# Kernel tuning notes

Hardware: AMD Instinct MI355X
Metric: run time of the kernel (lower is better)

Reference implementation:

```python
import jax, jax.numpy as jnp
import numpy as np

B, L, N = 16, 512, 512
DM, DS, NL, DFF = 512, 16, 2, 2048
DI = 2 * DM          # expand=2
DCONV = 4
DTR = DM // 16       # dt_rank
H = 96
EPS = 1e-5


def _ln(x, w, b):
    m = jnp.mean(x, -1, keepdims=True)
    v = jnp.mean((x - m) ** 2, -1, keepdims=True)
    return (x - m) / jnp.sqrt(v + EPS) * w + b


def _mamba_dir(x, in_w, in_b, conv_w, conv_b, xp_w, dt_w, dt_b, A_log, Dp, out_w, out_b):
    # x: (B, S, DM)
    Bb, S, _ = x.shape
    xz = x @ in_w.T + in_b                       # (B,S,2*DI)
    u, z = jnp.split(xz, 2, -1)
    uc = jnp.swapaxes(u, 1, 2)                   # (B,DI,S)
    uc = jax.lax.conv_general_dilated(uc, conv_w[:, None, :], (1,), [(DCONV - 1, 0)],
                                      feature_group_count=DI,
                                      dimension_numbers=('NCH', 'OIH', 'NCH'))
    u = jax.nn.silu(jnp.swapaxes(uc + conv_b[None, :, None], 1, 2))  # (B,S,DI)
    x_dbl = u @ xp_w.T                           # (B,S,DTR+2*DS)
    dt, Bm, Cm = jnp.split(x_dbl, [DTR, DTR + DS], -1)
    delta = jax.nn.softplus(dt @ dt_w.T + dt_b)  # (B,S,DI)
    A = -jnp.exp(A_log)                          # (DI,DS)

    def step(h, inp):
        u_t, d_t, B_t, C_t = inp                 # (B,DI),(B,DI),(B,DS),(B,DS)
        h = jnp.exp(d_t[:, :, None] * A) * h + (d_t * u_t)[:, :, None] * B_t[:, None, :]
        return h, jnp.einsum('bds,bs->bd', h, C_t)

    h0 = jnp.zeros((Bb, DI, DS), x.dtype)
    _, ys = jax.lax.scan(step, h0, (jnp.swapaxes(u, 0, 1), jnp.swapaxes(delta, 0, 1),
                                    jnp.swapaxes(Bm, 0, 1), jnp.swapaxes(Cm, 0, 1)))
    y = jnp.swapaxes(ys, 0, 1) + u * Dp          # (B,S,DI)
    y = y * jax.nn.silu(z)
    return y @ out_w.T + out_b                   # (B,S,DM)


def _forward(x, tok_w, tok_b, in_w, in_b, conv_w, conv_b, xp_w, dt_w, dt_b, A_log, Dm,
             out_w, out_b, mnorm_w, mnorm_b, fnorm_w, fnorm_b, ffn_w1, ffn_b1, ffn_w2,
             ffn_b2, norm_w, norm_b, head_w, head_b):
    # RevIN: per-instance stats over time dim, no affine
    mu = jnp.mean(x, 1, keepdims=True)           # (B,1,N)
    sd = jnp.sqrt(jnp.var(x, 1, keepdims=True) + EPS)
    xn = (x - mu) / sd
    tokens = jnp.swapaxes(xn, 1, 2) @ tok_w.T + tok_b   # (B,N,DM) variate tokens
    for l in range(NL):
        yn = _ln(tokens, mnorm_w[l], mnorm_b[l])
        of = _mamba_dir(yn, in_w[l, 0], in_b[l, 0], conv_w[l, 0], conv_b[l, 0], xp_w[l, 0],
                        dt_w[l, 0], dt_b[l, 0], A_log[l, 0], Dm[l, 0], out_w[l, 0], out_b[l, 0])
        ob = _mamba_dir(yn[:, ::-1, :], in_w[l, 1], in_b[l, 1], conv_w[l, 1], conv_b[l, 1],
                        xp_w[l, 1], dt_w[l, 1], dt_b[l, 1], A_log[l, 1], Dm[l, 1],
                        out_w[l, 1], out_b[l, 1])[:, ::-1, :]
        tokens = tokens + of + ob                # bidirectional Mamba + residual
        res = tokens
        hdd = _ln(tokens, fnorm_w[l], fnorm_b[l])
        hdd = jax.nn.gelu(hdd @ ffn_w1[l].T + ffn_b1[l]) @ ffn_w2[l].T + ffn_b2[l]
        tokens = hdd + res
    tokens = _ln(tokens, norm_w, norm_b)
    pred = tokens @ head_w.T + head_b            # (B,N,H)
    pred = jnp.swapaxes(pred, 1, 2)              # (B,H,N)
    return pred * sd + mu                        # RevIN inverse


def setup_inputs() -> dict:
    key = jax.random.key(0)
    ks = jax.random.split(key, 12)
    def rn(k, shape, scale=0.02):
        return jax.random.normal(k, shape, jnp.float32) * scale
    return {
        'x': jax.random.normal(ks[0], (B, L, N), jnp.float32),
        'tok_w': rn(ks[1], (DM, L)), 'tok_b': jnp.zeros((DM,), jnp.float32),
        'in_w': rn(ks[2], (NL, 2, 2 * DI, DM)), 'in_b': jnp.zeros((NL, 2, 2 * DI), jnp.float32),
        'conv_w': rn(ks[3], (NL, 2, DI, DCONV), 0.2), 'conv_b': jnp.zeros((NL, 2, DI), jnp.float32),
        'xp_w': rn(ks[4], (NL, 2, DTR + 2 * DS, DI)),
        'dt_w': rn(ks[5], (NL, 2, DI, DTR)), 'dt_b': rn(ks[6], (NL, 2, DI), 0.1),
        'A_log': jnp.broadcast_to(jnp.log(jnp.arange(1., DS + 1.)), (NL, 2, DI, DS)).astype(jnp.float32),
        'Dm': jnp.ones((NL, 2, DI), jnp.float32),
        'out_w': rn(ks[7], (NL, 2, DM, DI)), 'out_b': jnp.zeros((NL, 2, DM), jnp.float32),
        'mnorm_w': jnp.ones((NL, DM), jnp.float32), 'mnorm_b': jnp.zeros((NL, DM), jnp.float32),
        'fnorm_w': jnp.ones((NL, DM), jnp.float32), 'fnorm_b': jnp.zeros((NL, DM), jnp.float32),
        'ffn_w1': rn(ks[8], (NL, DFF, DM)), 'ffn_b1': jnp.zeros((NL, DFF), jnp.float32),
        'ffn_w2': rn(ks[9], (NL, DM, DFF)), 'ffn_b2': jnp.zeros((NL, DM), jnp.float32),
        'norm_w': jnp.ones((DM,), jnp.float32), 'norm_b': jnp.zeros((DM,), jnp.float32),
        'head_w': rn(ks[10], (H, DM)), 'head_b': jnp.zeros((H,), jnp.float32),
    }


def reference(x, tok_w, tok_b, in_w, in_b, conv_w, conv_b, xp_w, dt_w, dt_b, A_log, Dm,
              out_w, out_b, mnorm_w, mnorm_b, fnorm_w, fnorm_b, ffn_w1, ffn_b1, ffn_w2,
              ffn_b2, norm_w, norm_b, head_w, head_b):
    return _forward(x, tok_w, tok_b, in_w, in_b, conv_w, conv_b, xp_w, dt_w, dt_b, A_log,
                    Dm, out_w, out_b, mnorm_w, mnorm_b, fnorm_w, fnorm_b, ffn_w1, ffn_b1,
                    ffn_w2, ffn_b2, norm_w, norm_b, head_w, head_b)
```

## Files before the change

### kernel.cpp

```cpp
#include <hip/hip_runtime.h>
#include <hip/hip_bf16.h>

#define Bb 16
#define Ll 512
#define NV 512
#define DM 512
#define DS 16
#define NLAY 2
#define DFF 2048
#define DI 1024
#define DCONV 4
#define DTR 32
#define Hh 96
#define Ss NV
#define MROWS (Bb*Ss)
#define EPSf 1e-5f
#define CH 64
#define NCH (Ss/CH)

typedef __hip_bfloat16 bf16;
typedef __attribute__((ext_vector_type(8))) short bf16x8;
typedef __attribute__((ext_vector_type(4))) float f32x4;

#define GLL16(g, l) __builtin_amdgcn_global_load_lds( \
    (const __attribute__((address_space(1))) unsigned int*)(g), \
    (__attribute__((address_space(3))) unsigned int*)(l), 16, 0, 0)

__device__ __forceinline__ float fast_exp(float x) { return __expf(x); }
__device__ __forceinline__ float fast_sig(float x) {
    return __builtin_amdgcn_rcpf(1.f + __expf(-x));
}
__device__ __forceinline__ float fast_softplus(float r) {
    float e = __expf(-fabsf(r));
    return fmaxf(r, 0.f) + __logf(1.f + e);
}
__device__ __forceinline__ float b2f(bf16 v) { return __bfloat162float(v); }

__global__ void f2bf(const float* __restrict__ in, bf16* __restrict__ out, int n) {
    int i = (blockIdx.x * 256 + threadIdx.x) * 4;
    if (i < n) {
        float4 v = *(const float4*)(in + i);
        out[i + 0] = __float2bfloat16(v.x);
        out[i + 1] = __float2bfloat16(v.y);
        out[i + 2] = __float2bfloat16(v.z);
        out[i + 3] = __float2bfloat16(v.w);
    }
}

__global__ void repack_outw(const float* __restrict__ outw, bf16* __restrict__ outwcat) {
    int idx = (blockIdx.x * 256 + threadIdx.x) * 4;
    int k2 = idx & 2047;
    int rest = idx >> 11;
    int l = rest >> 9, n = rest & 511;
    int dirk = k2 >> 10, k = k2 & 1023;
    const float* s = outw + (((size_t)(l * 2 + dirk) * DM + n) * DI + k);
    float4 v = *(const float4*)s;
    bf16* dpt = outwcat + (size_t)idx;
    dpt[0] = __float2bfloat16(v.x);
    dpt[1] = __float2bfloat16(v.y);
    dpt[2] = __float2bfloat16(v.z);
    dpt[3] = __float2bfloat16(v.w);
}

__global__ void sum_outb(const float* __restrict__ outb, float* __restrict__ outbsum) {
    int i = blockIdx.x * 256 + threadIdx.x;
    int l = i >> 9, n = i & 511;
    outbsum[i] = outb[(l * 2 + 0) * DM + n] + outb[(l * 2 + 1) * DM + n];
}

__global__ void build_xpw2(const float* __restrict__ xpw, bf16* __restrict__ out) {
    int idx = blockIdx.x * 256 + threadIdx.x;
    int l = idx >> 18;
    int rest = idx & 262143;
    int n = rest >> 11, k = rest & 2047;
    int dir = n >> 6, nn = n & 63;
    float v = ((k >> 10) == dir) ? xpw[((size_t)(l * 2 + dir) * 64 + nn) * DI + (k & 1023)] : 0.f;
    out[idx] = __float2bfloat16(v);
}

__global__ void build_dtw2(const float* __restrict__ dtw, bf16* __restrict__ out) {
    int idx = blockIdx.x * 256 + threadIdx.x;
    int l = idx >> 18;
    int rest = idx & 262143;
    int n = rest >> 7, k = rest & 127;
    int dir = n >> 10, nn = n & 1023;
    int r = k - dir * 64;
    float v = (r >= 0 && r < DTR) ? dtw[((size_t)(l * 2 + dir) * DI + nn) * DTR + r] : 0.f;
    out[idx] = __float2bfloat16(v);
}

__global__ void revin_partial(const float* __restrict__ x, float* __restrict__ ps1,
                              float* __restrict__ ps2) {
    int b = blockIdx.x, c = blockIdx.y, n = threadIdx.x;
    const float* xp = x + (size_t)b * Ll * NV + (size_t)c * (Ll / 8) * NV + n;
    float s1 = 0.f, s2 = 0.f;
    #pragma unroll 4
    for (int l = 0; l < Ll / 8; l++) { float v = xp[(size_t)l * NV]; s1 += v; s2 += v * v; }
    ps1[((size_t)b * 8 + c) * NV + n] = s1;
    ps2[((size_t)b * 8 + c) * NV + n] = s2;
}

__global__ void revin_final(const float* __restrict__ ps1, const float* __restrict__ ps2,
                            float* __restrict__ mu, float* __restrict__ sd) {
    int b = blockIdx.x, n = threadIdx.x;
    float s1 = 0.f, s2 = 0.f;
    #pragma unroll
    for (int c = 0; c < 8; c++) {
        s1 += ps1[((size_t)b * 8 + c) * NV + n];
        s2 += ps2[((size_t)b * 8 + c) * NV + n];
    }
    float m = s1 / Ll;
    float var = s2 / Ll - m * m;
    mu[b * NV + n] = m;
    sd[b * NV + n] = sqrtf(var + EPSf);
}

__global__ void transpose_norm(const float* __restrict__ x, const float* __restrict__ mu,
                               const float* __restrict__ sd, bf16* __restrict__ xnT) {
    __shared__ float t[32][33];
    int b = blockIdx.z;
    int l0 = blockIdx.x * 32, n0 = blockIdx.y * 32;
    int tx = threadIdx.x, ty = threadIdx.y;
    #pragma unroll
    for (int q = 0; q < 4; q++)
        t[ty + q * 8][tx] = x[(size_t)b * Ll * NV + (size_t)(l0 + ty + q * 8) * NV + n0 + tx];
    __syncthreads();
    #pragma unroll
    for (int q = 0; q < 4; q++) {
        int n = n0 + ty + q * 8;
        float m = mu[b * NV + n], s = sd[b * NV + n];
        xnT[(size_t)b * NV * Ll + (size_t)n * Ll + l0 + tx] = __float2bfloat16((t[tx][ty + q * 8] - m) / s);
    }
}

__global__ void ln_rows(const float* __restrict__ in, const float* __restrict__ w,
                        const float* __restrict__ bvec, bf16* __restrict__ out) {
    int row = blockIdx.x;
    int tid = threadIdx.x;
    float v = in[(size_t)row * DM + tid];
    float s1 = v, s2 = v * v;
    #pragma unroll
    for (int o = 32; o > 0; o >>= 1) { s1 += __shfl_down(s1, o, 64); s2 += __shfl_down(s2, o, 64); }
    __shared__ float l1[8], l2[8];
    int wv = tid >> 6, ln = tid & 63;
    if (ln == 0) { l1[wv] = s1; l2[wv] = s2; }
    __syncthreads();
    if (tid == 0) {
        float a = 0.f, c = 0.f;
        #pragma unroll
        for (int i = 0; i < DM / 64; i++) { a += l1[i]; c += l2[i]; }
        l1[0] = a; l2[0] = c;
    }
    __syncthreads();
    float mean = l1[0] / DM;
    float var = l2[0] / DM - mean * mean;
    float inv = rsqrtf(var + EPSf);
    out[(size_t)row * DM + tid] = __float2bfloat16((v - mean) * inv * w[tid] + bvec[tid]);
}

template<int EPI, bool ACC, bool OUTBF>
__global__ __launch_bounds__(256) void gemm128(
    const bf16* __restrict__ A, int lda,
    const bf16* __restrict__ W,
    const float* __restrict__ bias,
    void* __restrict__ Cv, int ldc,
    int M, int Nn, int K) {
    __shared__ bf16 As[2][128 * 32];
    __shared__ bf16 Bs[2][128 * 32];
    int m0 = blockIdx.x * 128, n0 = blockIdx.y * 128;
    int tid = threadIdx.x;
    int w = tid >> 6, lane = tid & 63;
    int wm = (w >> 1) * 64, wn = (w & 1) * 64;
    f32x4 acc[4][4] = {};

    int srow = w * 32 + (lane >> 2);
    int sslot = (lane & 3) ^ ((lane >> 3) & 3);
    long arow0 = m0 + srow, arow1 = m0 + srow + 16;
    const char* agp0 = (const char*)(A + arow0 * (long)lda) + sslot * 16;
    const char* agp1 = (const char*)(A + arow1 * (long)lda) + sslot * 16;
    long wr0 = n0 + srow;      if (wr0 >= Nn) wr0 = Nn - 1;
    long wr1 = n0 + srow + 16; if (wr1 >= Nn) wr1 = Nn - 1;
    const char* wgp0 = (const char*)(W + wr0 * (long)K) + sslot * 16;
    const char* wgp1 = (const char*)(W + wr1 * (long)K) + sslot * 16;

    char* a0 = (char*)As[0]; char* a1 = (char*)As[1];
    char* b0 = (char*)Bs[0]; char* b1 = (char*)Bs[1];
    int dA0 = (w * 32) * 64, dA1 = (w * 32 + 16) * 64;

    int lrow = lane & 15;
    int salt = ((lane >> 4) ^ ((lane >> 1) & 3)) * 16;

    const int nk = K >> 5;
#define STG128(pa, pb, ko) do { \
        GLL16(agp0 + (size_t)(ko) * 64, pa + dA0); \
        GLL16(agp1 + (size_t)(ko) * 64, pa + dA1); \
        GLL16(wgp0 + (size_t)(ko) * 64, pb + dA0); \
        GLL16(wgp1 + (size_t)(ko) * 64, pb + dA1); } while (0)

    STG128(a0, b0, 0);
    __syncthreads();
    for (int t = 0; t < nk; ++t) {
        char* ac = (t & 1) ? a1 : a0;
        char* bc = (t & 1) ? b1 : b0;
        if (t + 1 < nk) {
            char* an = (t & 1) ? a0 : a1;
            char* bn = (t & 1) ? b0 : b1;
            STG128(an, bn, t + 1);
        }
        bf16x8 af[4], bfr[4];
        #pragma unroll
        for (int i = 0; i < 4; i++) {
            af[i]  = *(const bf16x8*)(ac + (wm + i * 16 + lrow) * 64 + salt);
            bfr[i] = *(const bf16x8*)(bc + (wn + i * 16 + lrow) * 64 + salt);
        }
        #pragma unroll
        for (int i = 0; i < 4; i++)
            #pragma unroll
            for (int j = 0; j < 4; j++)
                acc[i][j] = __builtin_amdgcn_mfma_f32_16x16x32_bf16(af[i], bfr[j], acc[i][j], 0, 0, 0);
        __syncthreads();
    }
#undef STG128

    #pragma unroll
    for (int i = 0; i < 4; i++) {
        #pragma unroll
        for (int j = 0; j < 4; j++) {
            int n = n0 + wn + j * 16 + (lane & 15);
            if (n >= Nn) continue;
            float bv = bias ? bias[n] : 0.f;
            #pragma unroll
            for (int r = 0; r < 4; r++) {
                long m = m0 + wm + i * 16 + (lane >> 4) * 4 + r;
                float v = acc[i][j][r] + bv;
                if (EPI == 1) {
                    float x3 = v * v * v;
                    v = 0.5f * v * (1.f + tanhf(0.7978845608028654f * (v + 0.044715f * x3)));
                }
                if (OUTBF) {
                    ((bf16*)Cv)[m * (long)ldc + n] = __float2bfloat16(v);
                } else if (ACC) {
                    ((float*)Cv)[m * (long)ldc + n] += v;
                } else {
                    ((float*)Cv)[m * (long)ldc + n] = v;
                }
            }
        }
    }
}

template<int EPI, bool ACC, bool OUTBF, int MT>
__global__ __launch_bounds__(256) void gemm64(
    const bf16* __restrict__ A, int lda,
    const bf16* __restrict__ W,
    const float* __restrict__ bias,
    void* __restrict__ Cv, int ldc,
    int M, int Nn, int K) {
    constexpr int WR = MT / 4;
    constexpr int IF = MT / 64;
    constexpr int AG = WR / 8;
    __shared__ bf16 As[2][MT * 64];
    __shared__ bf16 Bs[2][64 * 64];
    int m0 = blockIdx.x * MT, n0 = blockIdx.y * 64;
    int tid = threadIdx.x;
    int w = tid >> 6, lane = tid & 63;
    int wm = w * WR;
    f32x4 acc[IF][4] = {};

    int srow = lane >> 3;
    int sslot = (lane & 7) ^ srow;
    const char* agp[AG];
    #pragma unroll
    for (int g = 0; g < AG; g++) {
        long ar = m0 + w * WR + g * 8 + srow;
        agp[g] = (const char*)(A + ar * (long)lda) + sslot * 16;
    }
    const char* wgp[2];
    #pragma unroll
    for (int g = 0; g < 2; g++) {
        long br = n0 + w * 16 + g * 8 + srow;
        if (br >= Nn) br = Nn - 1;
        wgp[g] = (const char*)(W + br * (long)K) + sslot * 16;
    }
    char* a0 = (char*)As[0]; char* a1 = (char*)As[1];
    char* b0 = (char*)Bs[0]; char* b1 = (char*)Bs[1];

    int lrow = lane & 15;
    int rk = lane & 7, hi = lane >> 4;
    int salt0 = (hi ^ rk) * 16;
    int salt1 = ((4 + hi) ^ rk) * 16;

    const int nk = K >> 6;
#define STG64(pa, pb, ko) do { \
        _Pragma("unroll") \
        for (int g = 0; g < AG; g++) \
            GLL16(agp[g] + (size_t)(ko) * 128, pa + (w * WR + g * 8) * 128); \
        _Pragma("unroll") \
        for (int g = 0; g < 2; g++) \
            GLL16(wgp[g] + (size_t)(ko) * 128, pb + (w * 16 + g * 8) * 128); } while (0)

    STG64(a0, b0, 0);
    __syncthreads();
    for (int t = 0; t < nk; ++t) {
        char* ac = (t & 1) ? a1 : a0;
        char* bc = (t & 1) ? b1 : b0;
        if (t + 1 < nk) {
            char* an = (t & 1) ? a0 : a1;
            char* bn = (t & 1) ? b0 : b1;
            STG64(an, bn, t + 1);
        }
        bf16x8 af[2][IF], bfr[2][4];
        #pragma unroll
        for (int i = 0; i < IF; i++) {
            af[0][i] = *(const bf16x8*)(ac + (wm + i * 16 + lrow) * 128 + salt0);
            af[1][i] = *(const bf16x8*)(ac + (wm + i * 16 + lrow) * 128 + salt1);
        }
        #pragma unroll
        for (int j = 0; j < 4; j++) {
            bfr[0][j] = *(const bf16x8*)(bc + (j * 16 + lrow) * 128 + salt0);
            bfr[1][j] = *(const bf16x8*)(bc + (j * 16 + lrow) * 128 + salt1);
        }
        #pragma unroll
        for (int kk = 0; kk < 2; kk++)
            #pragma unroll
            for (int i = 0; i < IF; i++)
                #pragma unroll
                for (int j = 0; j < 4; j++)
                    acc[i][j] = __builtin_amdgcn_mfma_f32_16x16x32_bf16(af[kk][i], bfr[kk][j], acc[i][j], 0, 0, 0);
        __syncthreads();
    }
#undef STG64

    #pragma unroll
    for (int i = 0; i < IF; i++) {
        #pragma unroll
        for (int j = 0; j < 4; j++) {
            int n = n0 + j * 16 + (lane & 15);
            if (n >= Nn) continue;
            float bv = bias ? bias[n] : 0.f;
            #pragma unroll
            for (int r = 0; r < 4; r++) {
                long m = m0 + wm + i * 16 + (lane >> 4) * 4 + r;
                float v = acc[i][j][r] + bv;
                if (EPI == 1) {
                    float x3 = v * v * v;
                    v = 0.5f * v * (1.f + tanhf(0.7978845608028654f * (v + 0.044715f * x3)));
                } else if (EPI == 2) {
                    v = fast_softplus(v);
                }
                if (OUTBF) {
                    ((bf16*)Cv)[m * (long)ldc + n] = __float2bfloat16(v);
                } else if (ACC) {
                    ((float*)Cv)[m * (long)ldc + n] += v;
                } else {
                    ((float*)Cv)[m * (long)ldc + n] = v;
                }
            }
        }
    }
}

__global__ void conv_both(const bf16* __restrict__ xz, const float* __restrict__ cw_l,
                          const float* __restrict__ cb_l, bf16* __restrict__ ub) {
    int c2 = blockIdx.x * 256 + threadIdx.x;
    int dir = c2 >> 10, c = c2 & 1023;
    int s0 = blockIdx.y * 16;
    int b = blockIdx.z;
    const bf16* src = xz + (size_t)b * Ss * 4096 + (size_t)dir * 2048 + c;
    const float* cw = cw_l + (dir * DI + c) * 4;
    float w0 = cw[0], w1 = cw[1], w2 = cw[2], w3 = cw[3];
    float bias = cb_l[dir * DI + c];
    bf16* dst = ub + (size_t)b * Ss * 2048 + (size_t)dir * 1024 + c;
    if (dir == 0) {
        float r0 = (s0 - 3 >= 0) ? b2f(src[(size_t)(s0 - 3) * 4096]) : 0.f;
        float r1 = (s0 - 2 >= 0) ? b2f(src[(size_t)(s0 - 2) * 4096]) : 0.f;
        float r2 = (s0 - 1 >= 0) ? b2f(src[(size_t)(s0 - 1) * 4096]) : 0.f;
        for (int i = 0; i < 16; i++) {
            int s = s0 + i;
            float r3 = b2f(src[(size_t)s * 4096]);
            float a = fmaf(r0, w0, fmaf(r1, w1, fmaf(r2, w2, fmaf(r3, w3, bias))));
            dst[(size_t)s * 2048] = __float2bfloat16(a * fast_sig(a));
            r0 = r1; r1 = r2; r2 = r3;
        }
    } else {
        float f0 = b2f(src[(size_t)s0 * 4096]);
        float f1 = (s0 + 1 < Ss) ? b2f(src[(size_t)(s0 + 1) * 4096]) : 0.f;
        float f2 = (s0 + 2 < Ss) ? b2f(src[(size_t)(s0 + 2) * 4096]) : 0.f;
        float f3 = (s0 + 3 < Ss) ? b2f(src[(size_t)(s0 + 3) * 4096]) : 0.f;
        for (int i = 0; i < 16; i++) {
            int s = s0 + i;
            float a = fmaf(f0, w3, fmaf(f1, w2, fmaf(f2, w1, fmaf(f3, w0, bias))));
            dst[(size_t)s * 2048] = __float2bfloat16(a * fast_sig(a));
            f0 = f1; f1 = f2; f2 = f3;
            f3 = (s + 4 < Ss) ? b2f(src[(size_t)(s + 4) * 4096]) : 0.f;
        }
    }
}

__global__ __launch_bounds__(256) void scan_pass1(
    const bf16* __restrict__ delb,
    const bf16* __restrict__ ub,
    const float* __restrict__ xd,
    const float* __restrict__ Alog_l,
    float* __restrict__ PB, float* __restrict__ HB) {
    int d2 = blockIdx.x * 256 + threadIdx.x;
    int dir = d2 >> 10, d = d2 & 1023;
    int c = blockIdx.y;
    int b = blockIdx.z;
    float Aj[DS], h[DS];
    const float* al = Alog_l + ((size_t)dir * DI + d) * DS;
    #pragma unroll
    for (int j = 0; j < DS; j++) { Aj[j] = -fast_exp(al[j]); h[j] = 0.f; }
    float dlsum = 0.f;
    for (int i = 0; i < CH; i++) {
        int t = c * CH + i;
        int p = dir ? (Ss - 1 - t) : t;
        size_t row = (size_t)b * Ss + p;
        float dl = b2f(delb[row * 2048 + d2]);
        float ut = b2f(ub[row * 2048 + d2]);
        float du = dl * ut;
        dlsum += dl;
        const float4* q4 = (const float4*)(xd + row * 128 + dir * 64 + DTR);
        float4 B0 = q4[0], B1 = q4[1], B2 = q4[2], B3 = q4[3];
        float Bv[DS] = {B0.x, B0.y, B0.z, B0.w, B1.x, B1.y, B1.z, B1.w,
                        B2.x, B2.y, B2.z, B2.w, B3.x, B3.y, B3.z, B3.w};
        #pragma unroll
        for (int j = 0; j < DS; j++) {
            float a = fast_exp(dl * Aj[j]);
            h[j] = fmaf(a, h[j], du * Bv[j]);
        }
    }
    size_t base = ((size_t)(b * NCH + c) * DS) * 2048 + d2;
    #pragma unroll
    for (int j = 0; j < DS; j++) {
        PB[base + (size_t)j * 2048] = fast_exp(dlsum * Aj[j]);
        HB[base + (size_t)j * 2048] = h[j];
    }
}

__global__ __launch_bounds__(256) void scan_pass2(
    const float* PB, const float* HB, float* HIN) {
    int idx = blockIdx.x * 256 + threadIdx.x;
    int b = idx >> 15;
    int rem = idx & 32767;
    float h = 0.f;
    #pragma unroll
    for (int c = 0; c < NCH; c++) {
        size_t o = ((size_t)(b * NCH + c)) * 32768 + rem;
        float p = PB[o];
        float hl = HB[o];
        HIN[o] = h;
        h = fmaf(p, h, hl);
    }
}

__global__ __launch_bounds__(256) void scan_pass3(
    const bf16* __restrict__ delb,
    const bf16* __restrict__ ub,
    const float* __restrict__ xd,
    const bf16* __restrict__ xzb,
    const float* __restrict__ Alog_l, const float* __restrict__ Dm_l,
    const float* __restrict__ HIN,
    bf16* __restrict__ yb) {
    int d2 = blockIdx.x * 256 + threadIdx.x;
    int dir = d2 >> 10, d = d2 & 1023;
    int c = blockIdx.y;
    int b = blockIdx.z;
    float Aj[DS], h[DS];
    const float* al = Alog_l + ((size_t)dir * DI + d) * DS;
    size_t hbase = ((size_t)(b * NCH + c) * DS) * 2048 + d2;
    #pragma unroll
    for (int j = 0; j < DS; j++) {
        Aj[j] = -fast_exp(al[j]);
        h[j] = HIN[hbase + (size_t)j * 2048];
    }
    float Dd = Dm_l[dir * DI + d];
    for (int i = 0; i < CH; i++) {
        int t = c * CH + i;
        int p = dir ? (Ss - 1 - t) : t;
        size_t row = (size_t)b * Ss + p;
        float dl = b2f(delb[row * 2048 + d2]);
        float ut = b2f(ub[row * 2048 + d2]);
        float zz = b2f(xzb[row * 4096 + dir * 2048 + 1024 + d]);
        float du = dl * ut;
        const float4* q4 = (const float4*)(xd + row * 128 + dir * 64 + DTR);
        float4 B0 = q4[0], B1 = q4[1], B2 = q4[2], B3 = q4[3];
        float4 C0 = q4[4], C1 = q4[5], C2 = q4[6], C3 = q4[7];
        float Bv[DS] = {B0.x, B0.y, B0.z, B0.w, B1.x, B1.y, B1.z, B1.w,
                        B2.x, B2.y, B2.z, B2.w, B3.x, B3.y, B3.z, B3.w};
        float Cv[DS] = {C0.x, C0.y, C0.z, C0.w, C1.x, C1.y, C1.z, C1.w,
                        C2.x, C2.y, C2.z, C2.w, C3.x, C3.y, C3.z, C3.w};
        float acc = 0.f;
        #pragma unroll
        for (int j = 0; j < DS; j++) {
            float a = fast_exp(dl * Aj[j]);
            h[j] = fmaf(a, h[j], du * Bv[j]);
            acc = fmaf(h[j], Cv[j], acc);
        }
        float sg = fast_sig(zz);
        yb[row * 2048 + d2] = __float2bfloat16((acc + ut * Dd) * (zz * sg));
    }
}

__global__ void finalize_out(const float* __restrict__ pred, const float* __restrict__ mu,
                             const float* __restrict__ sd, float* __restrict__ out) {
    int n = threadIdx.x;
    int h = blockIdx.x;
    int b = blockIdx.y;
    out[((size_t)b * Hh + h) * NV + n] =
        pred[((size_t)b * NV + n) * Hh + h] * sd[b * NV + n] + mu[b * NV + n];
}

extern "C" void kernel_launch(void* const* d_in, const int* in_sizes, int n_in,
                              void* d_out, int out_size, void* d_ws, size_t ws_size,
                              hipStream_t stream) {
    const float* x     = (const float*)d_in[0];
    const float* tokw  = (const float*)d_in[1];
    const float* tokb  = (const float*)d_in[2];
    const float* in_w  = (const float*)d_in[3];
    const float* in_b  = (const float*)d_in[4];
    const float* convw = (const float*)d_in[5];
    const float* convb = (const float*)d_in[6];
    const float* xpw   = (const float*)d_in[7];
    const float* dtw   = (const float*)d_in[8];
    const float* dtb   = (const float*)d_in[9];
    const float* Alog  = (const float*)d_in[10];
    const float* Dm    = (const float*)d_in[11];
    const float* outw  = (const float*)d_in[12];
    const float* outb  = (const float*)d_in[13];
    const float* mnw   = (const float*)d_in[14];
    const float* mnb   = (const float*)d_in[15];
    const float* fnw   = (const float*)d_in[16];
    const float* fnb   = (const float*)d_in[17];
    const float* fw1   = (const float*)d_in[18];
    const float* fb1   = (const float*)d_in[19];
    const float* fw2   = (const float*)d_in[20];
    const float* fb2   = (const float*)d_in[21];
    const float* nw    = (const float*)d_in[22];
    const float* nb    = (const float*)d_in[23];
    const float* hw    = (const float*)d_in[24];
    const float* hb    = (const float*)d_in[25];

    float* ws = (float*)d_ws;
    float* MU   = ws;
    float* SD   = MU + Bb * NV;
    float* R1   = SD + Bb * NV;
    float* T    = R1 + 2 * 1024 * 1024;
    float* YNR  = T + 4 * 1024 * 1024;
    float* XZR  = YNR + 2 * 1024 * 1024;
    float* UBR  = XZR + 16 * 1024 * 1024;
    float* DELR = UBR + 8 * 1024 * 1024;
    float* PB   = DELR + 8 * 1024 * 1024;
    float* HB   = PB + 4 * 1024 * 1024;
    float* YBR  = HB + 4 * 1024 * 1024;
    float* WBF  = YBR + 8 * 1024 * 1024;

    bf16* XNTb = (bf16*)R1;
    float* XD  = R1;
    bf16* XDb  = (bf16*)(R1 + 1024 * 1024);
    bf16* YNb  = (bf16*)YNR;
    bf16* XZb  = (bf16*)XZR;
    bf16* Ub   = (bf16*)UBR;
    bf16* DELb = (bf16*)DELR;
    bf16* Yb   = (bf16*)YBR;
    float* HIN = PB;
    float* PRED = DELR;

    bf16* wb = (bf16*)WBF;
    bf16* tokwb  = wb;  wb += (size_t)DM * Ll;
    bf16* inwb   = wb;  wb += (size_t)NLAY * 2 * 2 * DI * DM;
    bf16* xpw2b  = wb;  wb += (size_t)NLAY * 128 * 2048;
    bf16* dtw2b  = wb;  wb += (size_t)NLAY * 2048 * 128;
    bf16* outwc  = wb;  wb += (size_t)NLAY * DM * 2 * DI;
    bf16* fw1b   = wb;  wb += (size_t)NLAY * DFF * DM;
    bf16* fw2b   = wb;  wb += (size_t)NLAY * DM * DFF;
    bf16* hwb    = wb;  wb += (size_t)Hh * DM;
    float* outbsum = (float*)wb;
    float* PS1   = outbsum + NLAY * DM;
    float* PS2   = PS1 + Bb * 8 * NV;

    f2bf<<<(DM * Ll) / 1024, 256, 0, stream>>>(tokw, tokwb, DM * Ll);
    f2bf<<<(NLAY * 2 * 2 * DI * DM) / 1024, 256, 0, stream>>>(in_w, inwb, NLAY * 2 * 2 * DI * DM);
    build_xpw2<<<(NLAY * 128 * 2048) / 256, 256, 0, stream>>>(xpw, xpw2b);
    build_dtw2<<<(NLAY * 2048 * 128) / 256, 256, 0, stream>>>(dtw, dtw2b);
    repack_outw<<<(NLAY * DM * 2 * DI) / 1024, 256, 0, stream>>>(outw, outwc);
    sum_outb<<<(NLAY * DM) / 256, 256, 0, stream>>>(outb, outbsum);
    f2bf<<<(NLAY * DFF * DM) / 1024, 256, 0, stream>>>(fw1, fw1b, NLAY * DFF * DM);
    f2bf<<<(NLAY * DM * DFF) / 1024, 256, 0, stream>>>(fw2, fw2b, NLAY * DM * DFF);
    f2bf<<<(Hh * DM) / 1024, 256, 0, stream>>>(hw, hwb, Hh * DM);

    revin_partial<<<dim3(Bb, 8), NV, 0, stream>>>(x, PS1, PS2);
    revin_final<<<Bb, NV, 0, stream>>>(PS1, PS2, MU, SD);
    transpose_norm<<<dim3(Ll / 32, NV / 32, Bb), dim3(32, 8), 0, stream>>>(x, MU, SD, XNTb);
    gemm64<0, false, false, 128><<<dim3(MROWS / 128, DM / 64), 256, 0, stream>>>(
        XNTb, Ll, tokwb, tokb, T, DM, MROWS, DM, Ll);

    for (int l = 0; l < NLAY; l++) {
        ln_rows<<<MROWS, DM, 0, stream>>>(T, mnw + l * DM, mnb + l * DM, YNb);
        gemm128<0, false, true><<<dim3(MROWS / 128, 4096 / 128), 256, 0, stream>>>(
            YNb, DM, inwb + (size_t)l * 2 * 2 * DI * DM, in_b + (size_t)l * 2 * 2 * DI,
            XZb, 4096, MROWS, 4096, DM);
        conv_both<<<dim3(8, Ss / 16, Bb), 256, 0, stream>>>(
            XZb, convw + (size_t)l * 2 * DI * DCONV, convb + (size_t)l * 2 * DI, Ub);
        gemm64<0, false, false, 64><<<dim3(MROWS / 64, 2), 256, 0, stream>>>(
            Ub, 2048, xpw2b + (size_t)l * 128 * 2048, nullptr, XD, 128, MROWS, 128, 2048);
        f2bf<<<(MROWS * 128) / 1024, 256, 0, stream>>>(XD, XDb, MROWS * 128);
        gemm64<2, false, true, 128><<<dim3(MROWS / 128, 2048 / 64), 256, 0, stream>>>(
            XDb, 128, dtw2b + (size_t)l * 2048 * 128, dtb + (size_t)l * 2 * DI,
            DELb, 2048, MROWS, 2048, 128);
        scan_pass1<<<dim3(2048 / 256, NCH, Bb), 256, 0, stream>>>(
            DELb, Ub, XD, Alog + (size_t)l * 2 * DI * DS, PB, HB);
        scan_pass2<<<(Bb * DS * 2048) / 256, 256, 0, stream>>>(PB, HB, HIN);
        scan_pass3<<<dim3(2048 / 256, NCH, Bb), 256, 0, stream>>>(
            DELb, Ub, XD, XZb, Alog + (size_t)l * 2 * DI * DS, Dm + (size_t)l * 2 * DI,
            HIN, Yb);
        gemm64<0, true, false, 128><<<dim3(MROWS / 128, DM / 64), 256, 0, stream>>>(
            Yb, 2 * DI, outwc + (size_t)l * DM * 2 * DI, outbsum + l * DM,
            T, DM, MROWS, DM, 2 * DI);
        ln_rows<<<MROWS, DM, 0, stream>>>(T, fnw + l * DM, fnb + l * DM, YNb);
        gemm128<1, false, true><<<dim3(MROWS / 128, DFF / 128), 256, 0, stream>>>(
            YNb, DM, fw1b + (size_t)l * DFF * DM, fb1 + l * DFF, XZb, DFF, MROWS, DFF, DM);
        gemm64<0, true, false, 128><<<dim3(MROWS / 128, DM / 64), 256, 0, stream>>>(
            XZb, DFF, fw2b + (size_t)l * DM * DFF, fb2 + l * DM, T, DM, MROWS, DM, DFF);
    }
    ln_rows<<<MROWS, DM, 0, stream>>>(T, nw, nb, YNb);
    gemm64<0, false, false, 64><<<dim3(MROWS / 64, 2), 256, 0, stream>>>(
        YNb, DM, hwb, hb, PRED, Hh, MROWS, Hh, DM);
    finalize_out<<<dim3(Hh, Bb), NV, 0, stream>>>(PRED, MU, SD, (float*)d_out);
}
```

Baseline: 931.7 us.

## Compute local scan outputs in pass1 and apply carry-in correction per row in pass3

```diff
diff --git a/kernel.cpp b/kernel.cpp
--- a/kernel.cpp
+++ b/kernel.cpp
@@ -45,6 +45,11 @@
         out[i + 2] = __float2bfloat16(v.z);
         out[i + 3] = __float2bfloat16(v.w);
     }
+}
+
+__global__ void a2negA(const float* __restrict__ alog, float* __restrict__ negA, int n) {
+    int i = blockIdx.x * 256 + threadIdx.x;
+    if (i < n) negA[i] = -fast_exp(alog[i]);
 }
 
 __global__ void repack_outw(const float* __restrict__ outw, bf16* __restrict__ outwcat) {
@@ -398,91 +403,35 @@
 }
 
 __global__ __launch_bounds__(256) void scan_pass1(
-    const bf16* __restrict__ delb,
-    const bf16* __restrict__ ub,
+    bf16* __restrict__ delb_dt,
+    bf16* __restrict__ ub_ypre,
     const float* __restrict__ xd,
-    const float* __restrict__ Alog_l,
+    const float* __restrict__ negA_l,
+    const float* __restrict__ Dm_l,
     float* __restrict__ PB, float* __restrict__ HB) {
     int d2 = blockIdx.x * 256 + threadIdx.x;
     int dir = d2 >> 10, d = d2 & 1023;
     int c = blockIdx.y;
     int b = blockIdx.z;
     float Aj[DS], h[DS];
-    const float* al = Alog_l + ((size_t)dir * DI + d) * DS;
-    #pragma unroll
-    for (int j = 0; j < DS; j++) { Aj[j] = -fast_exp(al[j]); h[j] = 0.f; }
+    const float4* na4 = (const float4*)(negA_l + ((size_t)dir * DI + d) * DS);
+    float4 A0 = na4[0], A1 = na4[1], A2 = na4[2], A3 = na4[3];
+    Aj[0]=A0.x; Aj[1]=A0.y; Aj[2]=A0.z; Aj[3]=A0.w;
+    Aj[4]=A1.x; Aj[5]=A1.y; Aj[6]=A1.z; Aj[7]=A1.w;
+    Aj[8]=A2.x; Aj[9]=A2.y; Aj[10]=A2.z; Aj[11]=A2.w;
+    Aj[12]=A3.x; Aj[13]=A3.y; Aj[14]=A3.z; Aj[15]=A3.w;
+    #pragma unroll
+    for (int j = 0; j < DS; j++) h[j] = 0.f;
+    float Dd = Dm_l[dir * DI + d];
     float dlsum = 0.f;
     for (int i = 0; i < CH; i++) {
         int t = c * CH + i;
         int p = dir ? (Ss - 1 - t) : t;
         size_t row = (size_t)b * Ss + p;
-        float dl = b2f(delb[row * 2048 + d2]);
-        float ut = b2f(ub[row * 2048 + d2]);
+        float dl = b2f(delb_dt[row * 2048 + d2]);
+        float ut = b2f(ub_ypre[row * 2048 + d2]);
         float du = dl * ut;
         dlsum += dl;
-        const float4* q4 = (const float4*)(xd + row * 128 + dir * 64 + DTR);
-        float4 B0 = q4[0], B1 = q4[1], B2 = q4[2], B3 = q4[3];
-        float Bv[DS] = {B0.x, B0.y, B0.z, B0.w, B1.x, B1.y, B1.z, B1.w,
-                        B2.x, B2.y, B2.z, B2.w, B3.x, B3.y, B3.z, B3.w};
-        #pragma unroll
-        for (int j = 0; j < DS; j++) {
-            float a = fast_exp(dl * Aj[j]);
-            h[j] = fmaf(a, h[j], du * Bv[j]);
-        }
-    }
-    size_t base = ((size_t)(b * NCH + c) * DS) * 2048 + d2;
-    #pragma unroll
-    for (int j = 0; j < DS; j++) {
-        PB[base + (size_t)j * 2048] = fast_exp(dlsum * Aj[j]);
-        HB[base + (size_t)j * 2048] = h[j];
-    }
-}
-
-__global__ __launch_bounds__(256) void scan_pass2(
-    const float* PB, const float* HB, float* HIN) {
-    int idx = blockIdx.x * 256 + threadIdx.x;
-    int b = idx >> 15;
-    int rem = idx & 32767;
-    float h = 0.f;
-    #pragma unroll
-    for (int c = 0; c < NCH; c++) {
-        size_t o = ((size_t)(b * NCH + c)) * 32768 + rem;
-        float p = PB[o];
-        float hl = HB[o];
-        HIN[o] = h;
-        h = fmaf(p, h, hl);
-    }
-}
-
-__global__ __launch_bounds__(256) void scan_pass3(
-    const bf16* __restrict__ delb,
-    const bf16* __restrict__ ub,
-    const float* __restrict__ xd,
-    const bf16* __restrict__ xzb,
-    const float* __restrict__ Alog_l, const float* __restrict__ Dm_l,
-    const float* __restrict__ HIN,
-    bf16* __restrict__ yb) {
-    int d2 = blockIdx.x * 256 + threadIdx.x;
-    int dir = d2 >> 10, d = d2 & 1023;
-    int c = blockIdx.y;
-    int b = blockIdx.z;
-    float Aj[DS], h[DS];
-    const float* al = Alog_l + ((size_t)dir * DI + d) * DS;
-    size_t hbase = ((size_t)(b * NCH + c) * DS) * 2048 + d2;
-    #pragma unroll
-    for (int j = 0; j < DS; j++) {
-        Aj[j] = -fast_exp(al[j]);
-        h[j] = HIN[hbase + (size_t)j * 2048];
-    }
-    float Dd = Dm_l[dir * DI + d];
-    for (int i = 0; i < CH; i++) {
-        int t = c * CH + i;
-        int p = dir ? (Ss - 1 - t) : t;
-        size_t row = (size_t)b * Ss + p;
-        float dl = b2f(delb[row * 2048 + d2]);
-        float ut = b2f(ub[row * 2048 + d2]);
-        float zz = b2f(xzb[row * 4096 + dir * 2048 + 1024 + d]);
-        float du = dl * ut;
         const float4* q4 = (const float4*)(xd + row * 128 + dir * 64 + DTR);
         float4 B0 = q4[0], B1 = q4[1], B2 = q4[2], B3 = q4[3];
         float4 C0 = q4[4], C1 = q4[5], C2 = q4[6], C3 = q4[7];
@@ -497,9 +446,65 @@
             h[j] = fmaf(a, h[j], du * Bv[j]);
             acc = fmaf(h[j], Cv[j], acc);
         }
-        float sg = fast_sig(zz);
-        yb[row * 2048 + d2] = __float2bfloat16((acc + ut * Dd) * (zz * sg));
-    }
+        ub_ypre[row * 2048 + d2] = __float2bfloat16(acc + ut * Dd);
+        delb_dt[row * 2048 + d2] = __float2bfloat16(dlsum);
+    }
+    size_t base = ((size_t)(b * NCH + c) * DS) * 2048 + d2;
+    #pragma unroll
+    for (int j = 0; j < DS; j++) {
+        PB[base + (size_t)j * 2048] = fast_exp(dlsum * Aj[j]);
+        HB[base + (size_t)j * 2048] = h[j];
+    }
+}
+
+__global__ __launch_bounds__(256) void scan_pass2(
+    const float* PB, const float* HB, float* HIN) {
+    int idx = blockIdx.x * 256 + threadIdx.x;
+    int b = idx >> 15;
+    int rem = idx & 32767;
+    float h = 0.f;
+    #pragma unroll
+    for (int c = 0; c < NCH; c++) {
+        size_t o = ((size_t)(b * NCH + c)) * 32768 + rem;
+        float p = PB[o];
+        float hl = HB[o];
+        HIN[o] = h;
+        h = fmaf(p, h, hl);
+    }
+}
+
+__global__ __launch_bounds__(256) void scan_pass3(
+    const bf16* __restrict__ dt,
+    bf16* __restrict__ ypre_y,
+    const float* __restrict__ xd,
+    const bf16* __restrict__ xzb,
+    const float* __restrict__ negA_l,
+    const float* __restrict__ HIN) {
+    int d2 = blockIdx.x * 256 + threadIdx.x;
+    int dir = d2 >> 10, d = d2 & 1023;
+    int srow = blockIdx.y;
+    int b = blockIdx.z;
+    size_t row = (size_t)b * Ss + srow;
+    int t = dir ? (Ss - 1 - srow) : srow;
+    int c = t >> 6;
+    const float4* na4 = (const float4*)(negA_l + ((size_t)dir * DI + d) * DS);
+    float4 A0 = na4[0], A1 = na4[1], A2 = na4[2], A3 = na4[3];
+    float Aj[DS] = {A0.x, A0.y, A0.z, A0.w, A1.x, A1.y, A1.z, A1.w,
+                    A2.x, A2.y, A2.z, A2.w, A3.x, A3.y, A3.z, A3.w};
+    const float4* q4 = (const float4*)(xd + row * 128 + dir * 64 + DTR);
+    float4 C0 = q4[4], C1 = q4[5], C2 = q4[6], C3 = q4[7];
+    float Cv[DS] = {C0.x, C0.y, C0.z, C0.w, C1.x, C1.y, C1.z, C1.w,
+                    C2.x, C2.y, C2.z, C2.w, C3.x, C3.y, C3.z, C3.w};
+    float D = b2f(dt[row * 2048 + d2]);
+    size_t hbase = ((size_t)(b * NCH + c) * DS) * 2048 + d2;
+    float corr = 0.f;
+    #pragma unroll
+    for (int j = 0; j < DS; j++) {
+        corr = fmaf(Cv[j] * fast_exp(Aj[j] * D), HIN[hbase + (size_t)j * 2048], corr);
+    }
+    float y = b2f(ypre_y[row * 2048 + d2]) + corr;
+    float zz = b2f(xzb[row * 4096 + dir * 2048 + 1024 + d]);
+    ypre_y[row * 2048 + d2] = __float2bfloat16(y * (zz * fast_sig(zz)));
 }
 
 __global__ void finalize_out(const float* __restrict__ pred, const float* __restrict__ mu,
@@ -552,8 +557,7 @@
     float* DELR = UBR + 8 * 1024 * 1024;
     float* PB   = DELR + 8 * 1024 * 1024;
     float* HB   = PB + 4 * 1024 * 1024;
-    float* YBR  = HB + 4 * 1024 * 1024;
-    float* WBF  = YBR + 8 * 1024 * 1024;
+    float* WBF  = PB + 16 * 1024 * 1024;
 
     bf16* XNTb = (bf16*)R1;
     float* XD  = R1;
@@ -562,8 +566,8 @@
     bf16* XZb  = (bf16*)XZR;
     bf16* Ub   = (bf16*)UBR;
     bf16* DELb = (bf16*)DELR;
-    bf16* Yb   = (bf16*)YBR;
     float* HIN = PB;
+    bf16* Yb   = Ub;
     float* PRED = DELR;
 
     bf16* wb = (bf16*)WBF;
@@ -576,7 +580,8 @@
     bf16* fw2b   = wb;  wb += (size_t)NLAY * DM * DFF;
     bf16* hwb    = wb;  wb += (size_t)Hh * DM;
     float* outbsum = (float*)wb;
-    float* PS1   = outbsum + NLAY * DM;
+    float* negA  = outbsum + NLAY * DM;
+    float* PS1   = negA + NLAY * 2 * DI * DS;
     float* PS2   = PS1 + Bb * 8 * NV;
 
     f2bf<<<(DM * Ll) / 1024, 256, 0, stream>>>(tokw, tokwb, DM * Ll);
@@ -588,6 +593,7 @@
     f2bf<<<(NLAY * DFF * DM) / 1024, 256, 0, stream>>>(fw1, fw1b, NLAY * DFF * DM);
     f2bf<<<(NLAY * DM * DFF) / 1024, 256, 0, stream>>>(fw2, fw2b, NLAY * DM * DFF);
     f2bf<<<(Hh * DM) / 1024, 256, 0, stream>>>(hw, hwb, Hh * DM);
+    a2negA<<<(NLAY * 2 * DI * DS) / 256, 256, 0, stream>>>(Alog, negA, NLAY * 2 * DI * DS);
 
     revin_partial<<<dim3(Bb, 8), NV, 0, stream>>>(x, PS1, PS2);
     revin_final<<<Bb, NV, 0, stream>>>(PS1, PS2, MU, SD);
@@ -609,11 +615,10 @@
             XDb, 128, dtw2b + (size_t)l * 2048 * 128, dtb + (size_t)l * 2 * DI,
             DELb, 2048, MROWS, 2048, 128);
         scan_pass1<<<dim3(2048 / 256, NCH, Bb), 256, 0, stream>>>(
-            DELb, Ub, XD, Alog + (size_t)l * 2 * DI * DS, PB, HB);
+            DELb, Ub, XD, negA + (size_t)l * 2 * DI * DS, Dm + (size_t)l * 2 * DI, PB, HB);
         scan_pass2<<<(Bb * DS * 2048) / 256, 256, 0, stream>>>(PB, HB, HIN);
-        scan_pass3<<<dim3(2048 / 256, NCH, Bb), 256, 0, stream>>>(
-            DELb, Ub, XD, XZb, Alog + (size_t)l * 2 * DI * DS, Dm + (size_t)l * 2 * DI,
-            HIN, Yb);
+        scan_pass3<<<dim3(2048 / 256, Ss, Bb), 256, 0, stream>>>(
+            DELb, Ub, XD, XZb, negA + (size_t)l * 2 * DI * DS, HIN);
         gemm64<0, true, false, 128><<<dim3(MROWS / 128, DM / 64), 256, 0, stream>>>(
             Yb, 2 * DI, outwc + (size_t)l * DM * 2 * DI, outbsum + l * DM,
             T, DM, MROWS, DM, 2 * DI);
```

Measured after the change: 1.019 ms. 9.3% more time.
